# Kernel optimization log

Hardware: AMD Instinct MI355X
Metric: run time of the kernel (lower is better)

## Reference

```python
import jax, jax.numpy as jnp
import numpy as np

N = 20000        # nodes per type (ant, user)
E = 400000       # edges per relation
F_IN = 128       # args.user_num -> input feature dim
H = 10           # attention heads
D1, D2 = 16, 32  # per-head out channels of HGT layers 1 and 2
H1, H2 = H * D1, H * D2  # 160, 320


def _segment_softmax(logit, dst, n):
    m = jax.ops.segment_max(logit, dst, num_segments=n)
    e = jnp.exp(logit - m[dst])
    s = jax.ops.segment_sum(e, dst, num_segments=n)
    return e / (s[dst] + 1e-16)


def _hgt_layer(x_a, x_u, ei_au, ea_au, ei_ua, ea_ua,
               kw, kb, qw, qb, vw, vb, arel, mrel, prel, ew, eb, alw, alb, D):
    # per-node-type K/Q/V projections, reshaped to [N, H, D]
    def proj(x, w, b, i):
        return (x @ w[i] + b[i]).reshape(x.shape[0], H, D)
    k_a, q_a, v_a = proj(x_a, kw, kb, 0), proj(x_a, qw, qb, 0), proj(x_a, vw, vb, 0)
    k_u, q_u, v_u = proj(x_u, kw, kb, 1), proj(x_u, qw, qb, 1), proj(x_u, vw, vb, 1)
    scale = 1.0 / jnp.sqrt(jnp.float32(D))

    def relation(k_s, v_s, q_d, ei, ea, r, n_dst):
        # apply per-relation matrices at node granularity (cheaper than per-edge)
        kr = jnp.einsum('nhd,hde->nhe', k_s, arel[r])
        vr = jnp.einsum('nhd,hde->nhe', v_s, mrel[r])
        src, dst = ei[0], ei[1]
        # [E, H] attention logits: HGT dot-product * relation prior + edge-attr term
        logit = (q_d[dst] * kr[src]).sum(-1) * scale * prel[r] + ea @ ew[r] + eb[r]
        a = _segment_softmax(logit, dst, n_dst)
        msg = vr[src] * a[..., None]                        # [E, H, D]
        out = jax.ops.segment_sum(msg, dst, num_segments=n_dst)
        return out.reshape(n_dst, H * D)

    agg_u = relation(k_a, v_a, q_u, ei_au, ea_au, 0, x_u.shape[0])  # ant -> user
    agg_a = relation(k_u, v_u, q_a, ei_ua, ea_ua, 1, x_a.shape[0])  # user -> ant
    out_a = jax.nn.gelu(agg_a) @ alw[0] + alb[0]
    out_u = jax.nn.gelu(agg_u) @ alw[1] + alb[1]
    return out_a, out_u


def _bn(x, g, b):
    mu = x.mean(0)
    var = x.var(0)
    return (x - mu) / jnp.sqrt(var + 1e-5) * g + b


def _forward(x_ant, x_user, ea_au, ea_ua,
             l1_kw, l1_kb, l1_qw, l1_qb, l1_vw, l1_vb, l1_arel, l1_mrel, l1_prel, l1_ew, l1_eb, l1_alw, l1_alb,
             l2_kw, l2_kb, l2_qw, l2_qb, l2_vw, l2_vb, l2_arel, l2_mrel, l2_prel, l2_ew, l2_eb, l2_alw, l2_alb,
             lin1_w, lin1_b, bn_g, bn_b, lin2_wa, lin2_ba, lin2_wu, lin2_bu,
             ei_au, ei_ua):
    a, u = _hgt_layer(x_ant, x_user, ei_au, ea_au, ei_ua, ea_ua,
                      l1_kw, l1_kb, l1_qw, l1_qb, l1_vw, l1_vb,
                      l1_arel, l1_mrel, l1_prel, l1_ew, l1_eb, l1_alw, l1_alb, D1)
    a, u = jax.nn.elu(a), jax.nn.elu(u)
    a, u = _hgt_layer(a, u, ei_au, ea_au, ei_ua, ea_ua,
                      l2_kw, l2_kb, l2_qw, l2_qb, l2_vw, l2_vb,
                      l2_arel, l2_mrel, l2_prel, l2_ew, l2_eb, l2_alw, l2_alb, D2)
    a, u = jax.nn.elu(a), jax.nn.elu(u)
    a = jax.nn.elu(a @ lin1_w[0] + lin1_b[0])
    u = jax.nn.elu(u @ lin1_w[1] + lin1_b[1])
    a = _bn(a, bn_g[0], bn_b[0])
    u = _bn(u, bn_g[1], bn_b[1])
    a = a @ lin2_wa + lin2_ba       # [N, user_num]   beamforming weights
    u = u @ lin2_wu + lin2_bu       # [N, user_num+1] assignment logits
    # MM_Dict_ACT: power-normalize ant outputs, softmax user assignments
    a = a / jnp.sqrt((a * a).sum(-1, keepdims=True) + 1e-12)
    u = jax.nn.softmax(u, axis=-1)
    return a, u


def setup_inputs() -> dict:
    key = jax.random.key(0)
    ks = iter(jax.random.split(key, 64))
    nk = lambda: next(ks)
    rn = lambda shape, s=0.05: jax.random.normal(nk(), shape, dtype=jnp.float32) * s
    inp = {}
    inp['x_ant'] = rn((N, F_IN), 1.0)
    inp['x_user'] = rn((N, F_IN), 1.0)
    inp['ea_au'] = jax.random.uniform(nk(), (E, 1), dtype=jnp.float32)
    inp['ea_ua'] = jax.random.uniform(nk(), (E, 1), dtype=jnp.float32)

    def hgt_params(p, fin, d):
        hd = H * d
        inp[p + 'kw'] = rn((2, fin, hd)); inp[p + 'kb'] = jnp.zeros((2, hd))
        inp[p + 'qw'] = rn((2, fin, hd)); inp[p + 'qb'] = jnp.zeros((2, hd))
        inp[p + 'vw'] = rn((2, fin, hd)); inp[p + 'vb'] = jnp.zeros((2, hd))
        inp[p + 'arel'] = rn((2, H, d, d), 0.2)
        inp[p + 'mrel'] = rn((2, H, d, d), 0.2)
        inp[p + 'prel'] = jnp.ones((2, H), dtype=jnp.float32)
        inp[p + 'ew'] = rn((2, 1, H)); inp[p + 'eb'] = jnp.zeros((2, H))
        inp[p + 'alw'] = rn((2, hd, hd)); inp[p + 'alb'] = jnp.zeros((2, hd))

    hgt_params('l1_', F_IN, D1)
    hgt_params('l2_', H1, D2)
    inp['lin1_w'] = rn((2, H2, 512)); inp['lin1_b'] = jnp.zeros((2, 512))
    inp['bn_g'] = jnp.ones((2, 512), dtype=jnp.float32)
    inp['bn_b'] = jnp.zeros((2, 512), dtype=jnp.float32)
    inp['lin2_wa'] = rn((512, F_IN)); inp['lin2_ba'] = jnp.zeros((F_IN,))
    inp['lin2_wu'] = rn((512, F_IN + 1)); inp['lin2_bu'] = jnp.zeros((F_IN + 1,))
    inp['ei_au'] = jax.random.randint(nk(), (2, E), 0, N)
    inp['ei_ua'] = jax.random.randint(nk(), (2, E), 0, N)
    return inp


def reference(x_ant, x_user, ea_au, ea_ua,
              l1_kw, l1_kb, l1_qw, l1_qb, l1_vw, l1_vb, l1_arel, l1_mrel, l1_prel, l1_ew, l1_eb, l1_alw, l1_alb,
              l2_kw, l2_kb, l2_qw, l2_qb, l2_vw, l2_vb, l2_arel, l2_mrel, l2_prel, l2_ew, l2_eb, l2_alw, l2_alb,
              lin1_w, lin1_b, bn_g, bn_b, lin2_wa, lin2_ba, lin2_wu, lin2_bu,
              ei_au, ei_ua):
    return _forward(x_ant, x_user, ea_au, ea_ua,
                    l1_kw, l1_kb, l1_qw, l1_qb, l1_vw, l1_vb, l1_arel, l1_mrel, l1_prel, l1_ew, l1_eb, l1_alw, l1_alb,
                    l2_kw, l2_kb, l2_qw, l2_qb, l2_vw, l2_vb, l2_arel, l2_mrel, l2_prel, l2_ew, l2_eb, l2_alw, l2_alb,
                    lin1_w, lin1_b, bn_g, bn_b, lin2_wa, lin2_ba, lin2_wu, lin2_bu,
                    ei_au, ei_ua)
```

## Files before the change

kernel.cpp:

```cpp
#include <hip/hip_runtime.h>
#include <hip/hip_bf16.h>
#include <math.h>

#define N_NODES 20000
#define N_EDGES 400000
#define NH 10

typedef __attribute__((ext_vector_type(8))) short short8v;
typedef __attribute__((ext_vector_type(4))) float f32x4;

__device__ __forceinline__ float gelu_f(float x) {
    float x3 = x * x * x;
    return 0.5f * x * (1.0f + tanhf(0.7978845608028654f * (x + 0.044715f * x3)));
}
__device__ __forceinline__ float elu_f(float x) {
    return x > 0.0f ? x : (expf(x) - 1.0f);
}
__device__ __forceinline__ float bf_lo(unsigned int w) {
    return __uint_as_float(w << 16);
}
__device__ __forceinline__ float bf_hi(unsigned int w) {
    return __uint_as_float(w & 0xffff0000u);
}
__device__ __forceinline__ unsigned short f2b(float x) {
    unsigned int u = __float_as_uint(x);
    return (unsigned short)((u + 0x7fffu + ((u >> 16) & 1u)) >> 16);
}

struct GemmPair {
    const __hip_bfloat16 *A0, *A1, *W0, *W1;
    const float *b0, *b1;
    void *C0, *C1;
    int N0, N1;
};
template<int ACT, typename OUT>
__global__ __launch_bounds__(256) void gemm2_kernel(GemmPair P, int M, int K)
{
    constexpr int PITCH = 40;
    __shared__ __align__(16) unsigned short As[128 * PITCH];
    __shared__ __align__(16) unsigned short Bs[128 * PITCH];
    const int z = blockIdx.z;
    const __hip_bfloat16* A  = z ? P.A1 : P.A0;
    const __hip_bfloat16* WT = z ? P.W1 : P.W0;
    const float* bias = z ? P.b1 : P.b0;
    OUT* C = (OUT*)(z ? P.C1 : P.C0);
    const int N = z ? P.N1 : P.N0;

    const int tid = threadIdx.x;
    const int m0 = blockIdx.y * 128, n0 = blockIdx.x * 128;
    if (n0 >= N) return;
    const int w = tid >> 6, l = tid & 63;
    const int wr = w >> 1, wc = w & 1;
    const int lr = l & 15, lk = l >> 4;

    const int srow = tid >> 1, sseg = (tid & 1) * 16;
    const bool ainb = (m0 + srow) < M;
    const bool binb = (n0 + srow) < N;
    const __hip_bfloat16* aptr = A + (size_t)(m0 + srow) * K + sseg;
    const __hip_bfloat16* bptr = WT + (size_t)(n0 + srow) * K + sseg;

    int4 ra0, ra1, rb0, rb1;
    auto ld = [&](int k0) {
        ra0 = ainb ? *reinterpret_cast<const int4*>(aptr + k0)     : make_int4(0, 0, 0, 0);
        ra1 = ainb ? *reinterpret_cast<const int4*>(aptr + k0 + 8) : make_int4(0, 0, 0, 0);
        rb0 = binb ? *reinterpret_cast<const int4*>(bptr + k0)     : make_int4(0, 0, 0, 0);
        rb1 = binb ? *reinterpret_cast<const int4*>(bptr + k0 + 8) : make_int4(0, 0, 0, 0);
    };

    f32x4 acc[4][4] = {};
    ld(0);
    for (int k0 = 0; k0 < K; k0 += 32) {
        *reinterpret_cast<int4*>(&As[srow * PITCH + sseg])     = ra0;
        *reinterpret_cast<int4*>(&As[srow * PITCH + sseg + 8]) = ra1;
        *reinterpret_cast<int4*>(&Bs[srow * PITCH + sseg])     = rb0;
        *reinterpret_cast<int4*>(&Bs[srow * PITCH + sseg + 8]) = rb1;
        __syncthreads();
        if (k0 + 32 < K) ld(k0 + 32);
        short8v a[4], b[4];
        #pragma unroll
        for (int mi = 0; mi < 4; ++mi)
            a[mi] = *reinterpret_cast<const short8v*>(
                &As[(wr * 64 + mi * 16 + lr) * PITCH + lk * 8]);
        #pragma unroll
        for (int ni = 0; ni < 4; ++ni)
            b[ni] = *reinterpret_cast<const short8v*>(
                &Bs[(wc * 64 + ni * 16 + lr) * PITCH + lk * 8]);
        #pragma unroll
        for (int mi = 0; mi < 4; ++mi)
            #pragma unroll
            for (int ni = 0; ni < 4; ++ni)
                acc[mi][ni] = __builtin_amdgcn_mfma_f32_16x16x32_bf16(
                    a[mi], b[ni], acc[mi][ni], 0, 0, 0);
        __syncthreads();
    }
    #pragma unroll
    for (int ni = 0; ni < 4; ++ni) {
        const int col = n0 + wc * 64 + ni * 16 + lr;
        if (col >= N) continue;
        const float bv = bias[col];
        #pragma unroll
        for (int mi = 0; mi < 4; ++mi) {
            const int rb = m0 + wr * 64 + mi * 16 + lk * 4;
            #pragma unroll
            for (int j = 0; j < 4; ++j) {
                const int m = rb + j;
                if (m >= M) continue;
                float v = acc[mi][ni][j] + bv;
                if (ACT == 1) v = elu_f(v);
                if constexpr (sizeof(OUT) == 2)
                    C[(size_t)m * N + col] = __float2bfloat16(v);
                else
                    C[(size_t)m * N + col] = v;
            }
        }
    }
}

struct TJob { const float* in; __hip_bfloat16* out; int K; int N; };
struct TJobs8 { TJob j[8]; };
__global__ void transpose8_kernel(TJobs8 J)
{
    __shared__ float tile[32][33];
    const TJob job = J.j[blockIdx.z];
    const int K = job.K, N = job.N;
    const int nb = blockIdx.x * 32, kb = blockIdx.y * 32;
    if (nb >= N || kb >= K) return;
    const int tx = threadIdx.x & 31, ty = threadIdx.x >> 5;
    for (int j = ty; j < 32; j += 8) {
        int k = kb + j, n = nb + tx;
        tile[j][tx] = (k < K && n < N) ? job.in[(size_t)k * N + n] : 0.f;
    }
    __syncthreads();
    for (int j = ty; j < 32; j += 8) {
        int n = nb + j, k = kb + tx;
        if (n < N && k < K) job.out[(size_t)n * K + k] = __float2bfloat16(tile[tx][j]);
    }
}

__global__ void convert_in_kernel(const float* __restrict__ in0, const float* __restrict__ in1,
                                  __hip_bfloat16* __restrict__ out0,
                                  __hip_bfloat16* __restrict__ out1, int n4)
{
    int i = blockIdx.x * blockDim.x + threadIdx.x;
    if (i >= n4) return;
    const float* in = blockIdx.y ? in1 : in0;
    __hip_bfloat16* out = blockIdx.y ? out1 : out0;
    float4 v = reinterpret_cast<const float4*>(in)[i];
    ushort4 b;
    b.x = f2b(v.x); b.y = f2b(v.y); b.z = f2b(v.z); b.w = f2b(v.w);
    reinterpret_cast<ushort4*>(out)[i] = b;
}

struct PrepArgs {
    const float *qw1, *qb1, *kw1, *kb1, *vw1, *vb1, *ar1, *mr1;
    const float *qw2, *qb2, *kw2, *kb2, *vw2, *vb2, *ar2, *mr2;
    __hip_bfloat16 *W1a, *W1u, *W2a, *W2u;
    float *B1a, *B1u, *B2a, *B2u;
};
__global__ void prep_qkv4_kernel(PrepArgs A)
{
    const int y = blockIdx.y;
    const int layer = y >> 1, type = y & 1;
    const int D = layer ? 32 : 16;
    const int fin = layer ? 160 : 128;
    const int HD = NH * D;
    const float* qw = layer ? A.qw2 : A.qw1;
    const float* qb = layer ? A.qb2 : A.qb1;
    const float* kw = layer ? A.kw2 : A.kw1;
    const float* kb = layer ? A.kb2 : A.kb1;
    const float* vw = layer ? A.vw2 : A.vw1;
    const float* vb = layer ? A.vb2 : A.vb1;
    const float* ar = layer ? A.ar2 : A.ar1;
    const float* mr = layer ? A.mr2 : A.mr1;
    __hip_bfloat16* WT = layer ? (type ? A.W2u : A.W2a) : (type ? A.W1u : A.W1a);
    float* BIAS = layer ? (type ? A.B2u : A.B2a) : (type ? A.B1u : A.B1a);
    const size_t woff = (size_t)type * fin * HD;
    const size_t roff = (size_t)type * NH * D * D;

    const int F1 = fin + 1;
    int tid = blockIdx.x * blockDim.x + threadIdx.x;
    if (tid >= 3 * HD * F1) return;
    const int f = tid % F1;
    const int col3 = tid / F1;
    const int sec = col3 / HD;
    const int col = col3 - sec * HD;
    float val;
    if (sec == 0) {
        val = (f < fin) ? qw[woff + (size_t)f * HD + col] : qb[type * HD + col];
    } else {
        const float* W = (sec == 1) ? kw : vw;
        const float* B = (sec == 1) ? kb : vb;
        const float* R = ((sec == 1) ? ar : mr) + roff;
        const int h = col / D, e = col - h * D;
        const float* src = (f < fin) ? W + woff + (size_t)f * HD + h * D
                                     : B + type * HD + h * D;
        const float* r = R + (size_t)h * D * D + e;
        float acc = 0.f;
        for (int d = 0; d < D; ++d) acc = fmaf(src[d], r[(size_t)d * D], acc);
        val = acc;
    }
    if (f < fin) WT[(size_t)col3 * fin + f] = __float2bfloat16(val);
    else         BIAS[col3] = val;
}

template<int D>
__global__ __launch_bounds__(256) void edge_fused_kernel(
    const __hip_bfloat16* __restrict__ Ta, const __hip_bfloat16* __restrict__ Tu,
    const int* __restrict__ rp0, const int* __restrict__ src0, const float* __restrict__ eav0,
    const int* __restrict__ rp1, const int* __restrict__ src1, const float* __restrict__ eav1,
    const float* __restrict__ prel, const float* __restrict__ ew,
    const float* __restrict__ eb,
    __hip_bfloat16* __restrict__ outA, __hip_bfloat16* __restrict__ outU,
    float scale)
{
    constexpr int HD = NH * D;
    constexpr int S = 3 * HD;
    constexpr int C = 64;
    constexpr int POS = HD / 8;
    constexpr int G = (POS * 8 <= 256) ? 8 : 4;
    __shared__ float q_s[HD];
    __shared__ float ls[C][NH];
    __shared__ int   srcs[C];
    __shared__ float eas[C];
    __shared__ float prel_s[NH], ew_s[NH], eb_s[NH];

    const int b = blockIdx.x;
    const int rel = b & 1, dst = b >> 1;
    const int t = threadIdx.x;
    const __hip_bfloat16* Tkv = rel ? Tu : Ta;
    const __hip_bfloat16* Tq  = rel ? Ta : Tu;
    const int* rp    = rel ? rp1 : rp0;
    const int* srcA  = rel ? src1 : src0;
    const float* eav = rel ? eav1 : eav0;
    __hip_bfloat16* out = rel ? outA : outU;

    const int s0 = rp[dst], deg = rp[dst + 1] - s0;

    {
        const unsigned int* qrow = (const unsigned int*)(Tq + (size_t)dst * S);
        for (int i = t; i < HD / 2; i += 256) {
            unsigned int wd = qrow[i];
            q_s[2 * i]     = bf_lo(wd);
            q_s[2 * i + 1] = bf_hi(wd);
        }
    }
    if (t < NH) { prel_s[t] = prel[rel * NH + t]; ew_s[t] = ew[rel * NH + t];
                  eb_s[t] = eb[rel * NH + t]; }
    const int apos = t / G, ag = t % G;
    const int ah = (apos * 8) / D;
    float a8[8] = {};
    float ssum = 0.f;
    __syncthreads();

    for (int base = 0; base < deg; base += C) {
        const int cl = min(C, deg - base);
        if (t < cl) {
            srcs[t] = srcA[s0 + base + t];
            eas[t]  = eav[s0 + base + t];
        }
        __syncthreads();
        for (int item = t; item < cl * NH; item += 256) {
            const int p = item / NH, h = item - p * NH;
            const uint4* kr = (const uint4*)(Tkv + (size_t)srcs[p] * S + HD + h * D);
            const float* qh = q_s + h * D;
            float d0 = 0.f;
            #pragma unroll
            for (int c4 = 0; c4 < D / 8; ++c4) {
                const uint4 wd = kr[c4];
                const float* qq = qh + c4 * 8;
                d0 = fmaf(qq[0], bf_lo(wd.x), d0); d0 = fmaf(qq[1], bf_hi(wd.x), d0);
                d0 = fmaf(qq[2], bf_lo(wd.y), d0); d0 = fmaf(qq[3], bf_hi(wd.y), d0);
                d0 = fmaf(qq[4], bf_lo(wd.z), d0); d0 = fmaf(qq[5], bf_hi(wd.z), d0);
                d0 = fmaf(qq[6], bf_lo(wd.w), d0); d0 = fmaf(qq[7], bf_hi(wd.w), d0);
            }
            ls[p][h] = expf(d0 * scale * prel_s[h] + eas[p] * ew_s[h] + eb_s[h]);
        }
        __syncthreads();
        if (apos < POS) {
            for (int p = ag; p < cl; p += G) {
                const uint4* vr = (const uint4*)(Tkv + (size_t)srcs[p] * S + 2 * HD);
                const uint4 wd = vr[apos];
                const float wgt = ls[p][ah];
                ssum += wgt;
                a8[0] = fmaf(wgt, bf_lo(wd.x), a8[0]); a8[1] = fmaf(wgt, bf_hi(wd.x), a8[1]);
                a8[2] = fmaf(wgt, bf_lo(wd.y), a8[2]); a8[3] = fmaf(wgt, bf_hi(wd.y), a8[3]);
                a8[4] = fmaf(wgt, bf_lo(wd.z), a8[4]); a8[5] = fmaf(wgt, bf_hi(wd.z), a8[5]);
                a8[6] = fmaf(wgt, bf_lo(wd.w), a8[6]); a8[7] = fmaf(wgt, bf_hi(wd.w), a8[7]);
            }
        }
        __syncthreads();
    }
    if (apos < POS) {
        #pragma unroll
        for (int off = G / 2; off; off >>= 1) {
            #pragma unroll
            for (int j = 0; j < 8; ++j) a8[j] += __shfl_xor(a8[j], off);
            ssum += __shfl_xor(ssum, off);
        }
        if (ag == 0) {
            const float inv = 1.f / (ssum + 1e-16f);
            uint4 o;
            o.x = (unsigned int)f2b(gelu_f(a8[0] * inv)) |
                  ((unsigned int)f2b(gelu_f(a8[1] * inv)) << 16);
            o.y = (unsigned int)f2b(gelu_f(a8[2] * inv)) |
                  ((unsigned int)f2b(gelu_f(a8[3] * inv)) << 16);
            o.z = (unsigned int)f2b(gelu_f(a8[4] * inv)) |
                  ((unsigned int)f2b(gelu_f(a8[5] * inv)) << 16);
            o.w = (unsigned int)f2b(gelu_f(a8[6] * inv)) |
                  ((unsigned int)f2b(gelu_f(a8[7] * inv)) << 16);
            ((uint4*)(out + (size_t)dst * HD))[apos] = o;
        }
    }
}

__global__ void count2_kernel(const int* __restrict__ ei0, const int* __restrict__ ei1,
                              int* __restrict__ cnt0, int* __restrict__ cnt1)
{
    int e = blockIdx.x * blockDim.x + threadIdx.x;
    if (e >= N_EDGES) return;
    if (blockIdx.y == 0) atomicAdd(&cnt0[ei0[N_EDGES + e]], 1);
    else                 atomicAdd(&cnt1[ei1[N_EDGES + e]], 1);
}

__global__ void scatter2_kernel(const int* __restrict__ ei0, const float* __restrict__ ea0,
                                const int* __restrict__ ei1, const float* __restrict__ ea1,
                                int* __restrict__ cur0, int* __restrict__ cur1,
                                int* __restrict__ srcA0, float* __restrict__ eaA0,
                                int* __restrict__ srcA1, float* __restrict__ eaA1)
{
    int e = blockIdx.x * blockDim.x + threadIdx.x;
    if (e >= N_EDGES) return;
    const int y = blockIdx.y;
    const int* ei = y ? ei1 : ei0;
    const float* ea = y ? ea1 : ea0;
    int* cursor = y ? cur1 : cur0;
    int* srcA = y ? srcA1 : srcA0;
    float* eaA = y ? eaA1 : eaA0;
    int dst = ei[N_EDGES + e];
    int pos = atomicAdd(&cursor[dst], 1);
    srcA[pos] = ei[e];
    eaA[pos] = ea[e];
}

__global__ void exscan2_kernel(const int* __restrict__ cnt0, int* __restrict__ rp0, int* __restrict__ cur0,
                               const int* __restrict__ cnt1, int* __restrict__ rp1, int* __restrict__ cur1,
                               int n)
{
    __shared__ int sums[1024];
    const int* cnt = blockIdx.x ? cnt1 : cnt0;
    int* rp = blockIdx.x ? rp1 : rp0;
    int* cursor = blockIdx.x ? cur1 : cur0;
    const int t = threadIdx.x;
    const int CH = (n + 1023) / 1024;
    const int b0 = t * CH;
    int local = 0;
    for (int i = 0; i < CH; ++i) {
        int idx = b0 + i;
        if (idx < n) local += cnt[idx];
    }
    sums[t] = local;
    __syncthreads();
    for (int off = 1; off < 1024; off <<= 1) {
        int x = (t >= off) ? sums[t - off] : 0;
        __syncthreads();
        sums[t] += x;
        __syncthreads();
    }
    int run = sums[t] - local;
    for (int i = 0; i < CH; ++i) {
        int idx = b0 + i;
        if (idx < n) {
            rp[idx] = run; cursor[idx] = run;
            run += cnt[idx];
        }
    }
    if (t == 1023) rp[n] = sums[1023];
}

__global__ void colstat2_kernel(const __hip_bfloat16* __restrict__ X0,
                                const __hip_bfloat16* __restrict__ X1,
                                float* __restrict__ sums, int M, int N)
{
    __shared__ float ls[256], lq[256];
    const int z = blockIdx.z;
    const __hip_bfloat16* X = z ? X1 : X0;
    float* sm = sums + z * 2 * N;
    int c = blockIdx.x * 64 + (threadIdx.x & 63);
    int rl = threadIdx.x >> 6;
    float s = 0.f, q = 0.f;
    for (int r = blockIdx.y * 4 + rl; r < M; r += gridDim.y * 4) {
        float v = __bfloat162float(X[(size_t)r * N + c]);
        s += v; q = fmaf(v, v, q);
    }
    ls[threadIdx.x] = s; lq[threadIdx.x] = q;
    __syncthreads();
    if (rl == 0) {
        s = ls[threadIdx.x] + ls[threadIdx.x + 64] + ls[threadIdx.x + 128] + ls[threadIdx.x + 192];
        q = lq[threadIdx.x] + lq[threadIdx.x + 64] + lq[threadIdx.x + 128] + lq[threadIdx.x + 192];
        atomicAdd(&sm[c], s);
        atomicAdd(&sm[N + c], q);
    }
}

__global__ void bn2_kernel(__hip_bfloat16* __restrict__ X0, __hip_bfloat16* __restrict__ X1,
                           const float* __restrict__ sums,
                           const float* __restrict__ g, const float* __restrict__ b,
                           int M, int N)
{
    int tid = blockIdx.x * blockDim.x + threadIdx.x;
    if (tid >= 2 * M * N) return;
    const int which = tid >= M * N;
    const int idx = tid - which * M * N;
    const int c = idx % N;
    __hip_bfloat16* X = which ? X1 : X0;
    const float* sm = sums + which * 2 * N;
    float mu = sm[c] / (float)M;
    float var = sm[N + c] / (float)M - mu * mu;
    float x = __bfloat162float(X[idx]);
    X[idx] = __float2bfloat16((x - mu) * rsqrtf(var + 1e-5f) * g[which * N + c]
                              + b[which * N + c]);
}

__global__ void epilogue_kernel(const float* __restrict__ XA, const float* __restrict__ XU,
                                float* __restrict__ out)
{
    const int row = blockIdx.x;
    const int l = threadIdx.x;
    if (blockIdx.y == 0) {
        const float* x = XA + (size_t)row * 128;
        float v0 = x[l], v1 = x[l + 64];
        float ss = v0 * v0 + v1 * v1;
        #pragma unroll
        for (int off = 32; off; off >>= 1) ss += __shfl_xor(ss, off);
        float inv = rsqrtf(ss + 1e-12f);
        out[(size_t)row * 128 + l] = v0 * inv;
        out[(size_t)row * 128 + l + 64] = v1 * inv;
    } else {
        const float* x = XU + (size_t)row * 129;
        float* o = out + (size_t)N_NODES * 128;
        float v0 = x[l], v1 = x[l + 64];
        float v2 = (l == 0) ? x[128] : -3.4e38f;
        float m = fmaxf(fmaxf(v0, v1), v2);
        #pragma unroll
        for (int off = 32; off; off >>= 1) m = fmaxf(m, __shfl_xor(m, off));
        float e0 = expf(v0 - m), e1 = expf(v1 - m);
        float e2 = (l == 0) ? expf(v2 - m) : 0.f;
        float s = e0 + e1 + e2;
        #pragma unroll
        for (int off = 32; off; off >>= 1) s += __shfl_xor(s, off);
        float inv = 1.f / s;
        o[(size_t)row * 129 + l] = e0 * inv;
        o[(size_t)row * 129 + l + 64] = e1 * inv;
        if (l == 0) o[(size_t)row * 129 + 128] = e2 * inv;
    }
}

template<int ACT, typename OUT>
static inline void launch_gemm2(const __hip_bfloat16* A0, const __hip_bfloat16* W0,
                                const float* b0, OUT* C0, int N0,
                                const __hip_bfloat16* A1, const __hip_bfloat16* W1,
                                const float* b1, OUT* C1, int N1,
                                int M, int K, hipStream_t s)
{
    GemmPair P = { A0, A1, W0, W1, b0, b1, (void*)C0, (void*)C1, N0, N1 };
    const int maxN = N0 > N1 ? N0 : N1;
    dim3 grid((maxN + 127) / 128, (M + 127) / 128, 2);
    gemm2_kernel<ACT, OUT><<<grid, 256, 0, s>>>(P, M, K);
}

struct LayerParams {
    const float *kw, *kb, *qw, *qb, *vw, *vb, *arel, *mrel, *prel, *ew, *eb, *alw, *alb;
};

struct CsrRel { const int* rp; const int* src; const float* eav; };

template<int D>
static void run_layer(const LayerParams& P, int fin,
                      const __hip_bfloat16* xa, const __hip_bfloat16* xu,
                      __hip_bfloat16* TA, __hip_bfloat16* TU,
                      __hip_bfloat16* AGA, __hip_bfloat16* AGU,
                      __hip_bfloat16* ya, __hip_bfloat16* yu,
                      const __hip_bfloat16* WQa, const __hip_bfloat16* WQu,
                      const float* Ba, const float* Bu,
                      const __hip_bfloat16* WALa, const __hip_bfloat16* WALu,
                      const CsrRel& au, const CsrRel& ua, hipStream_t s)
{
    const int HD = NH * D;
    const float scale = 1.0f / sqrtf((float)D);

    launch_gemm2<0, __hip_bfloat16>(xa, WQa, Ba, TA, 3 * HD,
                                    xu, WQu, Bu, TU, 3 * HD, N_NODES, fin, s);

    edge_fused_kernel<D><<<2 * N_NODES, 256, 0, s>>>(
        TA, TU, au.rp, au.src, au.eav, ua.rp, ua.src, ua.eav,
        P.prel, P.ew, P.eb, AGA, AGU, scale);

    launch_gemm2<1, __hip_bfloat16>(AGA, WALa, P.alb, ya, HD,
                                    AGU, WALu, P.alb + HD, yu, HD, N_NODES, HD, s);
}

extern "C" void kernel_launch(void* const* d_in, const int* in_sizes, int n_in,
                              void* d_out, int out_size, void* d_ws, size_t ws_size,
                              hipStream_t stream)
{
    const float* x_ant  = (const float*)d_in[0];
    const float* x_user = (const float*)d_in[1];
    const float* ea_au  = (const float*)d_in[2];
    const float* ea_ua  = (const float*)d_in[3];
    LayerParams L1 = {
        (const float*)d_in[4],  (const float*)d_in[5],  (const float*)d_in[6],
        (const float*)d_in[7],  (const float*)d_in[8],  (const float*)d_in[9],
        (const float*)d_in[10], (const float*)d_in[11], (const float*)d_in[12],
        (const float*)d_in[13], (const float*)d_in[14], (const float*)d_in[15],
        (const float*)d_in[16]
    };
    LayerParams L2 = {
        (const float*)d_in[17], (const float*)d_in[18], (const float*)d_in[19],
        (const float*)d_in[20], (const float*)d_in[21], (const float*)d_in[22],
        (const float*)d_in[23], (const float*)d_in[24], (const float*)d_in[25],
        (const float*)d_in[26], (const float*)d_in[27], (const float*)d_in[28],
        (const float*)d_in[29]
    };
    const float* lin1_w  = (const float*)d_in[30];
    const float* lin1_b  = (const float*)d_in[31];
    const float* bn_g    = (const float*)d_in[32];
    const float* bn_b    = (const float*)d_in[33];
    const float* lin2_wa = (const float*)d_in[34];
    const float* lin2_ba = (const float*)d_in[35];
    const float* lin2_wu = (const float*)d_in[36];
    const float* lin2_bu = (const float*)d_in[37];
    const int*   ei_au   = (const int*)d_in[38];
    const int*   ei_ua   = (const int*)d_in[39];

    char* P8 = (char*)d_ws;
    auto carve = [&](size_t bytes) { char* p = P8; P8 += (bytes + 255) & ~(size_t)255; return p; };
    __hip_bfloat16* XA  = (__hip_bfloat16*)carve((size_t)N_NODES * 128 * 2);
    __hip_bfloat16* XU  = (__hip_bfloat16*)carve((size_t)N_NODES * 128 * 2);
    __hip_bfloat16* TA  = (__hip_bfloat16*)carve((size_t)N_NODES * 960 * 2);
    __hip_bfloat16* TU  = (__hip_bfloat16*)carve((size_t)N_NODES * 960 * 2);
    __hip_bfloat16* AGA = (__hip_bfloat16*)carve((size_t)N_NODES * 320 * 2);
    __hip_bfloat16* AGU = (__hip_bfloat16*)carve((size_t)N_NODES * 320 * 2);
    __hip_bfloat16* YA  = (__hip_bfloat16*)carve((size_t)N_NODES * 320 * 2);
    __hip_bfloat16* YU  = (__hip_bfloat16*)carve((size_t)N_NODES * 320 * 2);
    __hip_bfloat16* L1A = (__hip_bfloat16*)carve((size_t)N_NODES * 512 * 2);
    __hip_bfloat16* L1U = (__hip_bfloat16*)carve((size_t)N_NODES * 512 * 2);
    __hip_bfloat16* WQ1A = (__hip_bfloat16*)carve(480 * 128 * 2);
    __hip_bfloat16* WQ1U = (__hip_bfloat16*)carve(480 * 128 * 2);
    __hip_bfloat16* WQ2A = (__hip_bfloat16*)carve(960 * 160 * 2);
    __hip_bfloat16* WQ2U = (__hip_bfloat16*)carve(960 * 160 * 2);
    __hip_bfloat16* WAL1A = (__hip_bfloat16*)carve(160 * 160 * 2);
    __hip_bfloat16* WAL1U = (__hip_bfloat16*)carve(160 * 160 * 2);
    __hip_bfloat16* WAL2A = (__hip_bfloat16*)carve(320 * 320 * 2);
    __hip_bfloat16* WAL2U = (__hip_bfloat16*)carve(320 * 320 * 2);
    __hip_bfloat16* WL1A = (__hip_bfloat16*)carve(512 * 320 * 2);
    __hip_bfloat16* WL1U = (__hip_bfloat16*)carve(512 * 320 * 2);
    __hip_bfloat16* WL2A = (__hip_bfloat16*)carve(128 * 512 * 2);
    __hip_bfloat16* WL2U = (__hip_bfloat16*)carve(129 * 512 * 2);
    float* B1A = (float*)carve(480 * 4);
    float* B1U = (float*)carve(480 * 4);
    float* B2A = (float*)carve(960 * 4);
    float* B2U = (float*)carve(960 * 4);
    float* STATS = (float*)carve(2048 * 4);
    int*   rp_au  = (int*)carve((N_NODES + 1) * 4);
    int*   rp_ua  = (int*)carve((N_NODES + 1) * 4);
    int*   src_au = (int*)carve((size_t)N_EDGES * 4);
    float* eav_au = (float*)carve((size_t)N_EDGES * 4);
    int*   src_ua = (int*)carve((size_t)N_EDGES * 4);
    float* eav_ua = (float*)carve((size_t)N_EDGES * 4);
    int*   cursor = (int*)carve((size_t)2 * N_NODES * 4);
    int*   counts = (int*)carve((size_t)2 * N_NODES * 4);

    const int gE = (N_EDGES + 255) / 256;

    {
        PrepArgs PA = {
            L1.qw, L1.qb, L1.kw, L1.kb, L1.vw, L1.vb, L1.arel, L1.mrel,
            L2.qw, L2.qb, L2.kw, L2.kb, L2.vw, L2.vb, L2.arel, L2.mrel,
            WQ1A, WQ1U, WQ2A, WQ2U, B1A, B1U, B2A, B2U
        };
        dim3 g((3 * 320 * 161 + 255) / 256, 4);
        prep_qkv4_kernel<<<g, 256, 0, stream>>>(PA);
    }
    {
        TJobs8 J = {{
            { L1.alw,                      WAL1A, 160, 160 },
            { L1.alw + (size_t)160 * 160,  WAL1U, 160, 160 },
            { L2.alw,                      WAL2A, 320, 320 },
            { L2.alw + (size_t)320 * 320,  WAL2U, 320, 320 },
            { lin1_w,                      WL1A,  320, 512 },
            { lin1_w + (size_t)320 * 512,  WL1U,  320, 512 },
            { lin2_wa,                     WL2A,  512, 128 },
            { lin2_wu,                     WL2U,  512, 129 }
        }};
        dim3 g(512 / 32, 512 / 32, 8);
        transpose8_kernel<<<g, 256, 0, stream>>>(J);
    }

    hipMemsetAsync(counts, 0, 2 * N_NODES * sizeof(int), stream);
    {
        dim3 g(gE, 2);
        count2_kernel<<<g, 256, 0, stream>>>(ei_au, ei_ua, counts, counts + N_NODES);
    }
    exscan2_kernel<<<2, 1024, 0, stream>>>(counts, rp_au, cursor,
                                           counts + N_NODES, rp_ua, cursor + N_NODES,
                                           N_NODES);
    {
        dim3 g(gE, 2);
        scatter2_kernel<<<g, 256, 0, stream>>>(ei_au, ea_au, ei_ua, ea_ua,
                                               cursor, cursor + N_NODES,
                                               src_au, eav_au, src_ua, eav_ua);
    }
    CsrRel au = { rp_au, src_au, eav_au };
    CsrRel ua = { rp_ua, src_ua, eav_ua };

    {
        dim3 g((N_NODES * 128 / 4 + 255) / 256, 2);
        convert_in_kernel<<<g, 256, 0, stream>>>(x_ant, x_user, XA, XU, N_NODES * 128 / 4);
    }

    run_layer<16>(L1, 128, XA, XU, TA, TU, AGA, AGU, YA, YU,
                  WQ1A, WQ1U, B1A, B1U, WAL1A, WAL1U, au, ua, stream);

    run_layer<32>(L2, 160, YA, YU, TA, TU, AGA, AGU, TA, TU,
                  WQ2A, WQ2U, B2A, B2U, WAL2A, WAL2U, au, ua, stream);

    launch_gemm2<1, __hip_bfloat16>(TA, WL1A, lin1_b, L1A, 512,
                                    TU, WL1U, lin1_b + 512, L1U, 512, N_NODES, 320, stream);

    hipMemsetAsync(STATS, 0, 2048 * sizeof(float), stream);
    {
        dim3 g(8, 32, 2);
        colstat2_kernel<<<g, 256, 0, stream>>>(L1A, L1U, STATS, N_NODES, 512);
    }
    bn2_kernel<<<(2 * N_NODES * 512 + 255) / 256, 256, 0, stream>>>(
        L1A, L1U, STATS, bn_g, bn_b, N_NODES, 512);

    float* OUTA = (float*)AGA;
    float* OUTU = (float*)AGU;
    launch_gemm2<0, float>(L1A, WL2A, lin2_ba, OUTA, 128,
                           L1U, WL2U, lin2_bu, OUTU, 129, N_NODES, 512, stream);
    {
        dim3 g(N_NODES, 2);
        epilogue_kernel<<<g, 64, 0, stream>>>(OUTA, OUTU, (float*)d_out);
    }
}
```

Baseline: 913.4 us.

## Fuse input conversion, BN statistics and BN apply into GEMM prologue/epilogue

The first QKV GEMM now reads the fp32 input directly and converts it to bf16 while staging into shared memory, which removes the separate convert kernel. The lin1 GEMM accumulates per-column sum and sum-of-squares in its epilogue through LDS and global atomics, replacing the colstat pass. A tiny kernel turns those sums into scale and shift, and the lin2 GEMM applies them while staging its A operand, replacing the bn2 pass. This saves several full passes over 20000x512 activations, at the cost of extra ALU and atomics inside the GEMMs and wider fp32 A loads.

```diff
diff --git a/kernel.cpp b/kernel.cpp
--- a/kernel.cpp
+++ b/kernel.cpp
@@ -27,20 +27,23 @@
     return (unsigned short)((u + 0x7fffu + ((u >> 16) & 1u)) >> 16);
 }
 
-struct GemmPair {
-    const __hip_bfloat16 *A0, *A1, *W0, *W1;
+struct GP {
+    const void *A0, *A1;
+    const __hip_bfloat16 *W0, *W1;
     const float *b0, *b1;
     void *C0, *C1;
     int N0, N1;
+    float* stats;
+    const float *scl, *sft;
 };
-template<int ACT, typename OUT>
-__global__ __launch_bounds__(256) void gemm2_kernel(GemmPair P, int M, int K)
+template<int ACT, int MODE, typename AT, typename OUT>
+__global__ __launch_bounds__(256) void gemm2_kernel(GP P, int M, int K)
 {
     constexpr int PITCH = 40;
     __shared__ __align__(16) unsigned short As[128 * PITCH];
     __shared__ __align__(16) unsigned short Bs[128 * PITCH];
     const int z = blockIdx.z;
-    const __hip_bfloat16* A  = z ? P.A1 : P.A0;
+    const AT* A  = (const AT*)(z ? P.A1 : P.A0);
     const __hip_bfloat16* WT = z ? P.W1 : P.W0;
     const float* bias = z ? P.b1 : P.b0;
     OUT* C = (OUT*)(z ? P.C1 : P.C0);
@@ -56,24 +59,54 @@
     const int srow = tid >> 1, sseg = (tid & 1) * 16;
     const bool ainb = (m0 + srow) < M;
     const bool binb = (n0 + srow) < N;
-    const __hip_bfloat16* aptr = A + (size_t)(m0 + srow) * K + sseg;
+    const AT* aptr = A + (size_t)(m0 + srow) * K + sseg;
     const __hip_bfloat16* bptr = WT + (size_t)(n0 + srow) * K + sseg;
 
-    int4 ra0, ra1, rb0, rb1;
+    constexpr int NRA = (sizeof(AT) == 4) ? 4 : 2;
+    int4 ra[NRA], rb0, rb1;
     auto ld = [&](int k0) {
-        ra0 = ainb ? *reinterpret_cast<const int4*>(aptr + k0)     : make_int4(0, 0, 0, 0);
-        ra1 = ainb ? *reinterpret_cast<const int4*>(aptr + k0 + 8) : make_int4(0, 0, 0, 0);
-        rb0 = binb ? *reinterpret_cast<const int4*>(bptr + k0)     : make_int4(0, 0, 0, 0);
-        rb1 = binb ? *reinterpret_cast<const int4*>(bptr + k0 + 8) : make_int4(0, 0, 0, 0);
+        #pragma unroll
+        for (int i = 0; i < NRA; ++i)
+            ra[i] = ainb ? ((const int4*)(aptr + k0))[i] : make_int4(0, 0, 0, 0);
+        rb0 = binb ? *(const int4*)(bptr + k0)     : make_int4(0, 0, 0, 0);
+        rb1 = binb ? *(const int4*)(bptr + k0 + 8) : make_int4(0, 0, 0, 0);
+    };
+    auto stage = [&](int k0) {
+        if constexpr (sizeof(AT) == 4) {
+            const float* fv = (const float*)ra;
+            unsigned int pk[8];
+            #pragma unroll
+            for (int q = 0; q < 8; ++q)
+                pk[q] = (unsigned int)f2b(fv[2 * q]) |
+                        ((unsigned int)f2b(fv[2 * q + 1]) << 16);
+            *(int4*)&As[srow * PITCH + sseg]     = *(int4*)&pk[0];
+            *(int4*)&As[srow * PITCH + sseg + 8] = *(int4*)&pk[4];
+        } else if constexpr (MODE == 2) {
+            const unsigned int* uv = (const unsigned int*)ra;
+            const float* scl = P.scl + z * 512;
+            const float* sft = P.sft + z * 512;
+            unsigned int pk[8];
+            #pragma unroll
+            for (int q = 0; q < 8; ++q) {
+                const int c0 = k0 + sseg + 2 * q;
+                float x0 = fmaf(bf_lo(uv[q]), scl[c0], sft[c0]);
+                float x1 = fmaf(bf_hi(uv[q]), scl[c0 + 1], sft[c0 + 1]);
+                pk[q] = (unsigned int)f2b(x0) | ((unsigned int)f2b(x1) << 16);
+            }
+            *(int4*)&As[srow * PITCH + sseg]     = *(int4*)&pk[0];
+            *(int4*)&As[srow * PITCH + sseg + 8] = *(int4*)&pk[4];
+        } else {
+            *(int4*)&As[srow * PITCH + sseg]     = ra[0];
+            *(int4*)&As[srow * PITCH + sseg + 8] = ra[1];
+        }
+        *(int4*)&Bs[srow * PITCH + sseg]     = rb0;
+        *(int4*)&Bs[srow * PITCH + sseg + 8] = rb1;
     };
 
     f32x4 acc[4][4] = {};
     ld(0);
     for (int k0 = 0; k0 < K; k0 += 32) {
-        *reinterpret_cast<int4*>(&As[srow * PITCH + sseg])     = ra0;
-        *reinterpret_cast<int4*>(&As[srow * PITCH + sseg + 8]) = ra1;
-        *reinterpret_cast<int4*>(&Bs[srow * PITCH + sseg])     = rb0;
-        *reinterpret_cast<int4*>(&Bs[srow * PITCH + sseg + 8]) = rb1;
+        stage(k0);
         __syncthreads();
         if (k0 + 32 < K) ld(k0 + 32);
         short8v a[4], b[4];
@@ -93,11 +126,18 @@
                     a[mi], b[ni], acc[mi][ni], 0, 0, 0);
         __syncthreads();
     }
+
+    float* cs = (float*)As;
+    if constexpr (MODE == 1) {
+        if (tid < 256) cs[tid] = 0.f;
+        __syncthreads();
+    }
     #pragma unroll
     for (int ni = 0; ni < 4; ++ni) {
         const int col = n0 + wc * 64 + ni * 16 + lr;
         if (col >= N) continue;
         const float bv = bias[col];
+        float lsum = 0.f, lsq = 0.f;
         #pragma unroll
         for (int mi = 0; mi < 4; ++mi) {
             const int rb = m0 + wr * 64 + mi * 16 + lk * 4;
@@ -107,13 +147,43 @@
                 if (m >= M) continue;
                 float v = acc[mi][ni][j] + bv;
                 if (ACT == 1) v = elu_f(v);
+                if constexpr (MODE == 1) { lsum += v; lsq = fmaf(v, v, lsq); }
                 if constexpr (sizeof(OUT) == 2)
                     C[(size_t)m * N + col] = __float2bfloat16(v);
                 else
                     C[(size_t)m * N + col] = v;
             }
         }
-    }
+        if constexpr (MODE == 1) {
+            const int ct = wc * 64 + ni * 16 + lr;
+            atomicAdd(&cs[ct], lsum);
+            atomicAdd(&cs[128 + ct], lsq);
+        }
+    }
+    if constexpr (MODE == 1) {
+        __syncthreads();
+        if (tid < 128) {
+            const int col = n0 + tid;
+            if (col < N) {
+                atomicAdd(&P.stats[z * 1024 + col], cs[tid]);
+                atomicAdd(&P.stats[z * 1024 + 512 + col], cs[128 + tid]);
+            }
+        }
+    }
+}
+
+__global__ void bnprep_kernel(const float* __restrict__ S, const float* __restrict__ g,
+                              const float* __restrict__ b,
+                              float* __restrict__ SCL, float* __restrict__ SFT)
+{
+    int t = blockIdx.x * 256 + threadIdx.x;
+    if (t >= 1024) return;
+    const int z = t >> 9, c = t & 511;
+    const float mu = S[z * 1024 + c] / (float)N_NODES;
+    const float var = S[z * 1024 + 512 + c] / (float)N_NODES - mu * mu;
+    const float scl = g[z * 512 + c] * rsqrtf(var + 1e-5f);
+    SCL[z * 512 + c] = scl;
+    SFT[z * 512 + c] = b[z * 512 + c] - mu * scl;
 }
 
 struct TJob { const float* in; __hip_bfloat16* out; int K; int N; };
@@ -135,20 +205,6 @@
         int n = nb + j, k = kb + tx;
         if (n < N && k < K) job.out[(size_t)n * K + k] = __float2bfloat16(tile[tx][j]);
     }
-}
-
-__global__ void convert_in_kernel(const float* __restrict__ in0, const float* __restrict__ in1,
-                                  __hip_bfloat16* __restrict__ out0,
-                                  __hip_bfloat16* __restrict__ out1, int n4)
-{
-    int i = blockIdx.x * blockDim.x + threadIdx.x;
-    if (i >= n4) return;
-    const float* in = blockIdx.y ? in1 : in0;
-    __hip_bfloat16* out = blockIdx.y ? out1 : out0;
-    float4 v = reinterpret_cast<const float4*>(in)[i];
-    ushort4 b;
-    b.x = f2b(v.x); b.y = f2b(v.y); b.z = f2b(v.z); b.w = f2b(v.w);
-    reinterpret_cast<ushort4*>(out)[i] = b;
 }
 
 struct PrepArgs {
@@ -377,50 +433,6 @@
     if (t == 1023) rp[n] = sums[1023];
 }
 
-__global__ void colstat2_kernel(const __hip_bfloat16* __restrict__ X0,
-                                const __hip_bfloat16* __restrict__ X1,
-                                float* __restrict__ sums, int M, int N)
-{
-    __shared__ float ls[256], lq[256];
-    const int z = blockIdx.z;
-    const __hip_bfloat16* X = z ? X1 : X0;
-    float* sm = sums + z * 2 * N;
-    int c = blockIdx.x * 64 + (threadIdx.x & 63);
-    int rl = threadIdx.x >> 6;
-    float s = 0.f, q = 0.f;
-    for (int r = blockIdx.y * 4 + rl; r < M; r += gridDim.y * 4) {
-        float v = __bfloat162float(X[(size_t)r * N + c]);
-        s += v; q = fmaf(v, v, q);
-    }
-    ls[threadIdx.x] = s; lq[threadIdx.x] = q;
-    __syncthreads();
-    if (rl == 0) {
-        s = ls[threadIdx.x] + ls[threadIdx.x + 64] + ls[threadIdx.x + 128] + ls[threadIdx.x + 192];
-        q = lq[threadIdx.x] + lq[threadIdx.x + 64] + lq[threadIdx.x + 128] + lq[threadIdx.x + 192];
-        atomicAdd(&sm[c], s);
-        atomicAdd(&sm[N + c], q);
-    }
-}
-
-__global__ void bn2_kernel(__hip_bfloat16* __restrict__ X0, __hip_bfloat16* __restrict__ X1,
-                           const float* __restrict__ sums,
-                           const float* __restrict__ g, const float* __restrict__ b,
-                           int M, int N)
-{
-    int tid = blockIdx.x * blockDim.x + threadIdx.x;
-    if (tid >= 2 * M * N) return;
-    const int which = tid >= M * N;
-    const int idx = tid - which * M * N;
-    const int c = idx % N;
-    __hip_bfloat16* X = which ? X1 : X0;
-    const float* sm = sums + which * 2 * N;
-    float mu = sm[c] / (float)M;
-    float var = sm[N + c] / (float)M - mu * mu;
-    float x = __bfloat162float(X[idx]);
-    X[idx] = __float2bfloat16((x - mu) * rsqrtf(var + 1e-5f) * g[which * N + c]
-                              + b[which * N + c]);
-}
-
 __global__ void epilogue_kernel(const float* __restrict__ XA, const float* __restrict__ XU,
                                 float* __restrict__ out)
 {
@@ -455,17 +467,20 @@
     }
 }
 
-template<int ACT, typename OUT>
-static inline void launch_gemm2(const __hip_bfloat16* A0, const __hip_bfloat16* W0,
+template<int ACT, int MODE, typename AT, typename OUT>
+static inline void launch_gemm2(const AT* A0, const __hip_bfloat16* W0,
                                 const float* b0, OUT* C0, int N0,
-                                const __hip_bfloat16* A1, const __hip_bfloat16* W1,
+                                const AT* A1, const __hip_bfloat16* W1,
                                 const float* b1, OUT* C1, int N1,
-                                int M, int K, hipStream_t s)
-{
-    GemmPair P = { A0, A1, W0, W1, b0, b1, (void*)C0, (void*)C1, N0, N1 };
+                                int M, int K, hipStream_t s,
+                                float* stats = nullptr,
+                                const float* scl = nullptr, const float* sft = nullptr)
+{
+    GP P = { (const void*)A0, (const void*)A1, W0, W1, b0, b1,
+             (void*)C0, (void*)C1, N0, N1, stats, scl, sft };
     const int maxN = N0 > N1 ? N0 : N1;
     dim3 grid((maxN + 127) / 128, (M + 127) / 128, 2);
-    gemm2_kernel<ACT, OUT><<<grid, 256, 0, s>>>(P, M, K);
+    gemm2_kernel<ACT, MODE, AT, OUT><<<grid, 256, 0, s>>>(P, M, K);
 }
 
 struct LayerParams {
@@ -474,9 +489,9 @@
 
 struct CsrRel { const int* rp; const int* src; const float* eav; };
 
-template<int D>
+template<int D, typename AT>
 static void run_layer(const LayerParams& P, int fin,
-                      const __hip_bfloat16* xa, const __hip_bfloat16* xu,
+                      const AT* xa, const AT* xu,
                       __hip_bfloat16* TA, __hip_bfloat16* TU,
                       __hip_bfloat16* AGA, __hip_bfloat16* AGU,
                       __hip_bfloat16* ya, __hip_bfloat16* yu,
@@ -488,15 +503,15 @@
     const int HD = NH * D;
     const float scale = 1.0f / sqrtf((float)D);
 
-    launch_gemm2<0, __hip_bfloat16>(xa, WQa, Ba, TA, 3 * HD,
-                                    xu, WQu, Bu, TU, 3 * HD, N_NODES, fin, s);
+    launch_gemm2<0, 0, AT, __hip_bfloat16>(xa, WQa, Ba, TA, 3 * HD,
+                                           xu, WQu, Bu, TU, 3 * HD, N_NODES, fin, s);
 
     edge_fused_kernel<D><<<2 * N_NODES, 256, 0, s>>>(
         TA, TU, au.rp, au.src, au.eav, ua.rp, ua.src, ua.eav,
         P.prel, P.ew, P.eb, AGA, AGU, scale);
 
-    launch_gemm2<1, __hip_bfloat16>(AGA, WALa, P.alb, ya, HD,
-                                    AGU, WALu, P.alb + HD, yu, HD, N_NODES, HD, s);
+    launch_gemm2<1, 0, __hip_bfloat16, __hip_bfloat16>(
+        AGA, WALa, P.alb, ya, HD, AGU, WALu, P.alb + HD, yu, HD, N_NODES, HD, s);
 }
 
 extern "C" void kernel_launch(void* const* d_in, const int* in_sizes, int n_in,
@@ -534,8 +549,6 @@
 
     char* P8 = (char*)d_ws;
     auto carve = [&](size_t bytes) { char* p = P8; P8 += (bytes + 255) & ~(size_t)255; return p; };
-    __hip_bfloat16* XA  = (__hip_bfloat16*)carve((size_t)N_NODES * 128 * 2);
-    __hip_bfloat16* XU  = (__hip_bfloat16*)carve((size_t)N_NODES * 128 * 2);
     __hip_bfloat16* TA  = (__hip_bfloat16*)carve((size_t)N_NODES * 960 * 2);
     __hip_bfloat16* TU  = (__hip_bfloat16*)carve((size_t)N_NODES * 960 * 2);
     __hip_bfloat16* AGA = (__hip_bfloat16*)carve((size_t)N_NODES * 320 * 2);
@@ -561,6 +574,8 @@
     float* B2A = (float*)carve(960 * 4);
     float* B2U = (float*)carve(960 * 4);
     float* STATS = (float*)carve(2048 * 4);
+    float* SCL = (float*)carve(1024 * 4);
+    float* SFT = (float*)carve(1024 * 4);
     int*   rp_au  = (int*)carve((N_NODES + 1) * 4);
     int*   rp_ua  = (int*)carve((N_NODES + 1) * 4);
     int*   src_au = (int*)carve((size_t)N_EDGES * 4);
@@ -597,6 +612,7 @@
     }
 
     hipMemsetAsync(counts, 0, 2 * N_NODES * sizeof(int), stream);
+    hipMemsetAsync(STATS, 0, 2048 * sizeof(float), stream);
     {
         dim3 g(gE, 2);
         count2_kernel<<<g, 256, 0, stream>>>(ei_au, ei_ua, counts, counts + N_NODES);
@@ -613,32 +629,23 @@
     CsrRel au = { rp_au, src_au, eav_au };
     CsrRel ua = { rp_ua, src_ua, eav_ua };
 
-    {
-        dim3 g((N_NODES * 128 / 4 + 255) / 256, 2);
-        convert_in_kernel<<<g, 256, 0, stream>>>(x_ant, x_user, XA, XU, N_NODES * 128 / 4);
-    }
-
-    run_layer<16>(L1, 128, XA, XU, TA, TU, AGA, AGU, YA, YU,
-                  WQ1A, WQ1U, B1A, B1U, WAL1A, WAL1U, au, ua, stream);
-
-    run_layer<32>(L2, 160, YA, YU, TA, TU, AGA, AGU, TA, TU,
-                  WQ2A, WQ2U, B2A, B2U, WAL2A, WAL2U, au, ua, stream);
-
-    launch_gemm2<1, __hip_bfloat16>(TA, WL1A, lin1_b, L1A, 512,
-                                    TU, WL1U, lin1_b + 512, L1U, 512, N_NODES, 320, stream);
-
-    hipMemsetAsync(STATS, 0, 2048 * sizeof(float), stream);
-    {
-        dim3 g(8, 32, 2);
-        colstat2_kernel<<<g, 256, 0, stream>>>(L1A, L1U, STATS, N_NODES, 512);
-    }
-    bn2_kernel<<<(2 * N_NODES * 512 + 255) / 256, 256, 0, stream>>>(
-        L1A, L1U, STATS, bn_g, bn_b, N_NODES, 512);
+    run_layer<16, float>(L1, 128, x_ant, x_user, TA, TU, AGA, AGU, YA, YU,
+                         WQ1A, WQ1U, B1A, B1U, WAL1A, WAL1U, au, ua, stream);
+
+    run_layer<32, __hip_bfloat16>(L2, 160, YA, YU, TA, TU, AGA, AGU, TA, TU,
+                                  WQ2A, WQ2U, B2A, B2U, WAL2A, WAL2U, au, ua, stream);
+
+    launch_gemm2<1, 1, __hip_bfloat16, __hip_bfloat16>(
+        TA, WL1A, lin1_b, L1A, 512, TU, WL1U, lin1_b + 512, L1U, 512,
+        N_NODES, 320, stream, STATS);
+
+    bnprep_kernel<<<4, 256, 0, stream>>>(STATS, bn_g, bn_b, SCL, SFT);
 
     float* OUTA = (float*)AGA;
     float* OUTU = (float*)AGU;
-    launch_gemm2<0, float>(L1A, WL2A, lin2_ba, OUTA, 128,
-                           L1U, WL2U, lin2_bu, OUTU, 129, N_NODES, 512, stream);
+    launch_gemm2<0, 2, __hip_bfloat16, float>(
+        L1A, WL2A, lin2_ba, OUTA, 128, L1U, WL2U, lin2_bu, OUTU, 129,
+        N_NODES, 512, stream, nullptr, SCL, SFT);
     {
         dim3 g(N_NODES, 2);
         epilogue_kernel<<<g, 64, 0, stream>>>(OUTA, OUTU, (float*)d_out);
```

Result: faster. 862.0 us (-5.6%).
